# Kernel tuning notes

Measured on AMD Instinct MI355X. Metric: run time of the kernel, lower is better.

Reference implementation:

```python
import jax, jax.numpy as jnp
import numpy as np

THRESH = 230.0   # options['dist_threshold'][0]
NCAT = 21        # options['supervised_categories']


def setup_inputs() -> dict:
    key = jax.random.key(0)
    k1, k2, k3 = jax.random.split(key, 3)
    b, N, d, T = 8, 16384, 128, 64  # N = h*w = 128*128
    frame_embeddings = jax.random.normal(k1, (b, N, d), dtype=jnp.float32)
    templates = jax.random.normal(k2, (T, N, d), dtype=jnp.float32)
    template_classes = jax.random.randint(k3, (T,), 0, 20, dtype=jnp.int64)
    return {"frame_embeddings": frame_embeddings, "templates": templates,
            "template_classes": template_classes}


def _min_dists(frame_embeddings, templates):
    # frame_embeddings: [b, n, d]; templates: [t, n, d]
    x2 = jnp.sum(frame_embeddings * frame_embeddings, axis=-1)          # [b, n]
    t2 = jnp.sum(templates * templates, axis=-1)                        # [t, n]
    xt = jnp.einsum('bnd,tnd->btn', frame_embeddings, templates)        # [b, t, n]
    dists = x2[:, None, :] - 2.0 * xt + t2[None, :, :]                  # [b, t, n]
    min_d = jnp.min(dists, axis=1)                                      # [b, n]
    min_idx = jnp.argmin(dists, axis=1)                                 # [b, n]
    return min_d, min_idx


def reference(frame_embeddings, templates, template_classes):
    b, N, _ = frame_embeddings.shape
    min_d, min_idx = _min_dists(frame_embeddings, templates)
    neigh_classes = template_classes[min_idx]                           # [b, n]
    mask = min_d <= THRESH                                              # [b, n] bool
    one_hot = jax.nn.one_hot(neigh_classes, NCAT, dtype=jnp.float32)    # [b, n, ncat]
    masked_pred = one_hot * mask[:, :, None].astype(jnp.float32)        # [b, n, ncat]
    neigh_classes_masked = jnp.where(mask, neigh_classes, NCAT - 1)     # [b, n]
    return (masked_pred, mask, neigh_classes_masked, min_d, neigh_classes)
```

## Files before the change

kernel.cpp:

```cpp
#include <hip/hip_runtime.h>


#define NPIX   16384
#define DDIM   128
#define NT     64
#define NB     8
#define NCAT   21
#define THRESH 230.0f
#define P      16
#define TSTR   132

__global__ __launch_bounds__(256, 4) void nn_openset_kernel(
    const float* __restrict__ frame,
    const float* __restrict__ tmpl,
    const int*   __restrict__ tcls,
    float* __restrict__ out)
{
    __shared__ __align__(16) float ts[2][P * TSTR];

    const int tid = threadIdx.x;
    const int n0  = blockIdx.x * P;

    const int bp = tid >> 6;
    const int ln = tid & 63;
    const int np = ln >> 2;
    const int dq = ln & 3;
    const int b0 = bp * 2, b1 = b0 + 1;
    const int n  = n0 + np;

    const int r0 = tid >> 5;
    const int c0 = tid & 31;
    const int w0 = r0 * TSTR + c0 * 4;
    const int w1 = (r0 + 8) * TSTR + c0 * 4;

    const size_t PLANE4 = (size_t)NPIX * (DDIM / 4);
    const float4* gq = (const float4*)tmpl + (size_t)n0 * (DDIM / 4);

    float4 s0 = gq[tid];
    float4 s1 = gq[tid + 256];
    gq += PLANE4;

    float4 fr0[8], fr1[8];
    {
        const float4* f0 = (const float4*)(frame + ((size_t)b0 * NPIX + n) * DDIM + dq * 32);
        const float4* f1 = (const float4*)(frame + ((size_t)b1 * NPIX + n) * DDIM + dq * 32);
        #pragma unroll
        for (int j = 0; j < 8; ++j) { fr0[j] = f0[j]; fr1[j] = f1[j]; }
    }

    *(float4*)(&ts[0][w0]) = s0;
    *(float4*)(&ts[0][w1]) = s1;
    __syncthreads();

    float vmin0 = 3.402823466e38f, vmin1 = 3.402823466e38f;
    int   imin0 = 0, imin1 = 0;

    for (int t = 0; t < NT; ++t) {
        if (t < NT - 1) { s0 = gq[tid]; s1 = gq[tid + 256]; gq += PLANE4; }

        const float* tsp = &ts[t & 1][np * TSTR + dq * 32];
        float a0 = 0.0f, a1 = 0.0f;
        #pragma unroll
        for (int kq = 0; kq < 8; ++kq) {
            const float4 tv = *(const float4*)(tsp + (kq << 2));
            const float4 x0 = fr0[kq];
            const float4 x1 = fr1[kq];
            float d;
            d = x0.x - tv.x; a0 = fmaf(d, d, a0);
            d = x0.y - tv.y; a0 = fmaf(d, d, a0);
            d = x0.z - tv.z; a0 = fmaf(d, d, a0);
            d = x0.w - tv.w; a0 = fmaf(d, d, a0);
            d = x1.x - tv.x; a1 = fmaf(d, d, a1);
            d = x1.y - tv.y; a1 = fmaf(d, d, a1);
            d = x1.z - tv.z; a1 = fmaf(d, d, a1);
            d = x1.w - tv.w; a1 = fmaf(d, d, a1);
        }
        a0 += __shfl_xor(a0, 1);
        a0 += __shfl_xor(a0, 2);
        a1 += __shfl_xor(a1, 1);
        a1 += __shfl_xor(a1, 2);

        const bool u0 = a0 < vmin0;
        const bool u1 = a1 < vmin1;
        imin0 = u0 ? t : imin0;  vmin0 = u0 ? a0 : vmin0;
        imin1 = u1 ? t : imin1;  vmin1 = u1 ? a1 : vmin1;

        if (t < NT - 1) {
            float* wp = ts[(t + 1) & 1];
            *(float4*)(&wp[w0]) = s0;
            *(float4*)(&wp[w1]) = s1;
        }
        __syncthreads();
    }

    const int  cls0 = tcls[imin0];
    const int  cls1 = tcls[imin1];
    const bool m0 = (vmin0 <= THRESH);
    const bool m1 = (vmin1 <= THRESH);

    float* o0 = out;
    float* o1 = out + (size_t)NB * NPIX * NCAT;
    float* o2 = o1 + NB * NPIX;
    float* o3 = o2 + NB * NPIX;
    float* o4 = o3 + NB * NPIX;

    const size_t p0 = (size_t)b0 * NPIX + n;
    const size_t p1 = (size_t)b1 * NPIX + n;

    if (dq == 0)      { o1[p0] = m0 ? 1.0f : 0.0f;          o1[p1] = m1 ? 1.0f : 0.0f; }
    else if (dq == 1) { o2[p0] = m0 ? (float)cls0 : 20.0f;  o2[p1] = m1 ? (float)cls1 : 20.0f; }
    else if (dq == 2) { o3[p0] = vmin0;                     o3[p1] = vmin1; }
    else              { o4[p0] = (float)cls0;               o4[p1] = (float)cls1; }

    #pragma unroll
    for (int j = 0; j < 6; ++j) {
        const int c = dq * 6 + j;
        if (c < NCAT) {
            o0[p0 * NCAT + c] = (m0 && c == cls0) ? 1.0f : 0.0f;
            o0[p1 * NCAT + c] = (m1 && c == cls1) ? 1.0f : 0.0f;
        }
    }
}

extern "C" void kernel_launch(void* const* d_in, const int* in_sizes, int n_in,
                              void* d_out, int out_size, void* d_ws, size_t ws_size,
                              hipStream_t stream) {
    const float* frame = (const float*)d_in[0];
    const float* tmpl  = (const float*)d_in[1];
    const int*   tcls  = (const int*)d_in[2];
    float* outp = (float*)d_out;
    nn_openset_kernel<<<NPIX / P, 256, 0, stream>>>(frame, tmpl, tcls, outp);
}
```

Measured before the change: 710.0 us.

## Stream templates into LDS via async global_load_lds with 4-stage ring buffer

Replaces the register-staged double-buffered template copy with direct global-to-LDS DMA loads (global_load_lds) into a 4-deep ring buffer, prefetching three templates ahead. An XOR swizzle on the source column replaces the padded stride to avoid LDS bank conflicts, and explicit vmcnt waits plus raw s_barrier replace __syncthreads. This aims to hide global-memory latency and cut the VGPR traffic of staging loads, at the cost of more LDS (32KB per block), which may limit occupancy, and fragile hand-tuned waitcnt counts.

```diff
diff --git a/kernel.cpp b/kernel.cpp
--- a/kernel.cpp
+++ b/kernel.cpp
@@ -8,7 +8,15 @@
 #define NCAT   21
 #define THRESH 230.0f
 #define P      16
-#define TSTR   132
+
+typedef float4 f4;
+
+__device__ __forceinline__ void dma16(const float* g, float* l) {
+    __builtin_amdgcn_global_load_lds(
+        (const __attribute__((address_space(1))) void*)g,
+        (__attribute__((address_space(3))) void*)l,
+        16 , 0, 0);
+}
 
 __global__ __launch_bounds__(256, 4) void nn_openset_kernel(
     const float* __restrict__ frame,
@@ -16,7 +24,7 @@
     const int*   __restrict__ tcls,
     float* __restrict__ out)
 {
-    __shared__ __align__(16) float ts[2][P * TSTR];
+    __shared__ __align__(16) float ts[4][P * DDIM];
 
     const int tid = threadIdx.x;
     const int n0  = blockIdx.x * P;
@@ -27,44 +35,58 @@
     const int dq = ln & 3;
     const int b0 = bp * 2, b1 = b0 + 1;
     const int n  = n0 + np;
+    const int wv = __builtin_amdgcn_readfirstlane(bp);
 
-    const int r0 = tid >> 5;
-    const int c0 = tid & 31;
-    const int w0 = r0 * TSTR + c0 * 4;
-    const int w1 = (r0 + 8) * TSTR + c0 * 4;
-
-    const size_t PLANE4 = (size_t)NPIX * (DDIM / 4);
-    const float4* gq = (const float4*)tmpl + (size_t)n0 * (DDIM / 4);
-
-    float4 s0 = gq[tid];
-    float4 s1 = gq[tid + 256];
-    gq += PLANE4;
-
-    float4 fr0[8], fr1[8];
+    f4 fr0[8], fr1[8];
     {
-        const float4* f0 = (const float4*)(frame + ((size_t)b0 * NPIX + n) * DDIM + dq * 32);
-        const float4* f1 = (const float4*)(frame + ((size_t)b1 * NPIX + n) * DDIM + dq * 32);
+        const f4* f0 = (const f4*)(frame + ((size_t)b0 * NPIX + n) * DDIM + dq * 32);
+        const f4* f1 = (const f4*)(frame + ((size_t)b1 * NPIX + n) * DDIM + dq * 32);
         #pragma unroll
         for (int j = 0; j < 8; ++j) { fr0[j] = f0[j]; fr1[j] = f1[j]; }
     }
 
-    *(float4*)(&ts[0][w0]) = s0;
-    *(float4*)(&ts[0][w1]) = s1;
-    __syncthreads();
+    const size_t PLANE = (size_t)NPIX * DDIM;
+    const int c0  = tid;
+    const int c1  = tid + 256;
+    const int sc0 = c0 ^ ((c0 >> 5) & 7);
+    const int sc1 = c1 ^ ((c1 >> 5) & 7);
+    const float* gp0 = tmpl + (size_t)n0 * DDIM + sc0 * 4;
+    const float* gp1 = tmpl + (size_t)n0 * DDIM + sc1 * 4;
+    const int ldso0 = wv * 256;
+    const int ldso1 = 1024 + wv * 256;
+
+    dma16(gp0,             &ts[0][ldso0]);  dma16(gp1,             &ts[0][ldso1]);
+    dma16(gp0 + PLANE,     &ts[1][ldso0]);  dma16(gp1 + PLANE,     &ts[1][ldso1]);
+    dma16(gp0 + 2 * PLANE, &ts[2][ldso0]);  dma16(gp1 + 2 * PLANE, &ts[2][ldso1]);
+    gp0 += 3 * PLANE;  gp1 += 3 * PLANE;
+
+    const int s  = np & 7;
+    const int rb = np * DDIM + dq * 32;
+    int roff[8];
+    #pragma unroll
+    for (int kq = 0; kq < 8; ++kq) roff[kq] = rb + ((kq ^ s) << 2);
+
+    asm volatile("s_waitcnt vmcnt(4)" ::: "memory");
+    __builtin_amdgcn_s_barrier();
 
     float vmin0 = 3.402823466e38f, vmin1 = 3.402823466e38f;
     int   imin0 = 0, imin1 = 0;
 
     for (int t = 0; t < NT; ++t) {
-        if (t < NT - 1) { s0 = gq[tid]; s1 = gq[tid + 256]; gq += PLANE4; }
+        if (t + 3 < NT) {
+            float* wb = ts[(t + 3) & 3];
+            dma16(gp0, wb + ldso0);
+            dma16(gp1, wb + ldso1);
+            gp0 += PLANE;  gp1 += PLANE;
+        }
 
-        const float* tsp = &ts[t & 1][np * TSTR + dq * 32];
+        const float* tb = ts[t & 3];
         float a0 = 0.0f, a1 = 0.0f;
         #pragma unroll
         for (int kq = 0; kq < 8; ++kq) {
-            const float4 tv = *(const float4*)(tsp + (kq << 2));
-            const float4 x0 = fr0[kq];
-            const float4 x1 = fr1[kq];
+            const f4 tv = *(const f4*)(tb + roff[kq]);
+            const f4 x0 = fr0[kq];
+            const f4 x1 = fr1[kq];
             float d;
             d = x0.x - tv.x; a0 = fmaf(d, d, a0);
             d = x0.y - tv.y; a0 = fmaf(d, d, a0);
@@ -75,10 +97,8 @@
             d = x1.z - tv.z; a1 = fmaf(d, d, a1);
             d = x1.w - tv.w; a1 = fmaf(d, d, a1);
         }
-        a0 += __shfl_xor(a0, 1);
-        a0 += __shfl_xor(a0, 2);
-        a1 += __shfl_xor(a1, 1);
-        a1 += __shfl_xor(a1, 2);
+        a0 += __shfl_xor(a0, 1);  a0 += __shfl_xor(a0, 2);
+        a1 += __shfl_xor(a1, 1);  a1 += __shfl_xor(a1, 2);
 
         const bool u0 = a0 < vmin0;
         const bool u1 = a1 < vmin1;
@@ -86,11 +106,11 @@
         imin1 = u1 ? t : imin1;  vmin1 = u1 ? a1 : vmin1;
 
         if (t < NT - 1) {
-            float* wp = ts[(t + 1) & 1];
-            *(float4*)(&wp[w0]) = s0;
-            *(float4*)(&wp[w1]) = s1;
+            if (t < NT - 3)       asm volatile("s_waitcnt vmcnt(4)" ::: "memory");
+            else if (t == NT - 3) asm volatile("s_waitcnt vmcnt(2)" ::: "memory");
+            else                  asm volatile("s_waitcnt vmcnt(0)" ::: "memory");
+            __builtin_amdgcn_s_barrier();
         }
-        __syncthreads();
     }
 
     const int  cls0 = tcls[imin0];
```

Result: no change. 717.5 us (+1.0%).

## Drop LDS template staging; load templates directly from global per thread

Applied to the files above, without the earlier changes.

Removes the double-buffered shared-memory staging of template rows and the per-iteration block barrier. The thread mapping changes so that the four batch lanes sharing a pixel read the same template data directly from global memory, relying on L1/L2 broadcast. This removes synchronisation and LDS traffic but gives up explicit prefetch overlap, and it raises register pressure by holding 8 float4 template values per iteration.

```diff
diff --git a/kernel.cpp b/kernel.cpp
--- a/kernel.cpp
+++ b/kernel.cpp
@@ -8,7 +8,8 @@
 #define NCAT   21
 #define THRESH 230.0f
 #define P      16
-#define TSTR   132
+
+typedef float4 f4;
 
 __global__ __launch_bounds__(256, 4) void nn_openset_kernel(
     const float* __restrict__ frame,
@@ -16,81 +17,60 @@
     const int*   __restrict__ tcls,
     float* __restrict__ out)
 {
-    __shared__ __align__(16) float ts[2][P * TSTR];
-
     const int tid = threadIdx.x;
     const int n0  = blockIdx.x * P;
 
-    const int bp = tid >> 6;
+    const int wv = tid >> 6;
     const int ln = tid & 63;
-    const int np = ln >> 2;
+    const int np = ln >> 4;
+    const int b  = (ln >> 2) & 3;
     const int dq = ln & 3;
-    const int b0 = bp * 2, b1 = b0 + 1;
-    const int n  = n0 + np;
+    const int n  = n0 + wv * 4 + np;
+    const int b0 = b, b1 = b + 4;
 
-    const int r0 = tid >> 5;
-    const int c0 = tid & 31;
-    const int w0 = r0 * TSTR + c0 * 4;
-    const int w1 = (r0 + 8) * TSTR + c0 * 4;
-
-    const size_t PLANE4 = (size_t)NPIX * (DDIM / 4);
-    const float4* gq = (const float4*)tmpl + (size_t)n0 * (DDIM / 4);
-
-    float4 s0 = gq[tid];
-    float4 s1 = gq[tid + 256];
-    gq += PLANE4;
-
-    float4 fr0[8], fr1[8];
+    f4 fr0[8], fr1[8];
     {
-        const float4* f0 = (const float4*)(frame + ((size_t)b0 * NPIX + n) * DDIM + dq * 32);
-        const float4* f1 = (const float4*)(frame + ((size_t)b1 * NPIX + n) * DDIM + dq * 32);
+        const f4* f0 = (const f4*)(frame + ((size_t)b0 * NPIX + n) * DDIM + dq * 32);
+        const f4* f1 = (const f4*)(frame + ((size_t)b1 * NPIX + n) * DDIM + dq * 32);
         #pragma unroll
         for (int j = 0; j < 8; ++j) { fr0[j] = f0[j]; fr1[j] = f1[j]; }
     }
 
-    *(float4*)(&ts[0][w0]) = s0;
-    *(float4*)(&ts[0][w1]) = s1;
-    __syncthreads();
+    const size_t PLANE4 = (size_t)NPIX * (DDIM / 4);
+    const f4* tp = (const f4*)tmpl + (size_t)n * (DDIM / 4) + dq * 8;
 
     float vmin0 = 3.402823466e38f, vmin1 = 3.402823466e38f;
     int   imin0 = 0, imin1 = 0;
 
     for (int t = 0; t < NT; ++t) {
-        if (t < NT - 1) { s0 = gq[tid]; s1 = gq[tid + 256]; gq += PLANE4; }
+        f4 tv[8];
+        #pragma unroll
+        for (int kq = 0; kq < 8; ++kq) tv[kq] = tp[kq];
+        tp += PLANE4;
 
-        const float* tsp = &ts[t & 1][np * TSTR + dq * 32];
         float a0 = 0.0f, a1 = 0.0f;
         #pragma unroll
         for (int kq = 0; kq < 8; ++kq) {
-            const float4 tv = *(const float4*)(tsp + (kq << 2));
-            const float4 x0 = fr0[kq];
-            const float4 x1 = fr1[kq];
+            const f4 v  = tv[kq];
+            const f4 x0 = fr0[kq];
+            const f4 x1 = fr1[kq];
             float d;
-            d = x0.x - tv.x; a0 = fmaf(d, d, a0);
-            d = x0.y - tv.y; a0 = fmaf(d, d, a0);
-            d = x0.z - tv.z; a0 = fmaf(d, d, a0);
-            d = x0.w - tv.w; a0 = fmaf(d, d, a0);
-            d = x1.x - tv.x; a1 = fmaf(d, d, a1);
-            d = x1.y - tv.y; a1 = fmaf(d, d, a1);
-            d = x1.z - tv.z; a1 = fmaf(d, d, a1);
-            d = x1.w - tv.w; a1 = fmaf(d, d, a1);
+            d = x0.x - v.x; a0 = fmaf(d, d, a0);
+            d = x0.y - v.y; a0 = fmaf(d, d, a0);
+            d = x0.z - v.z; a0 = fmaf(d, d, a0);
+            d = x0.w - v.w; a0 = fmaf(d, d, a0);
+            d = x1.x - v.x; a1 = fmaf(d, d, a1);
+            d = x1.y - v.y; a1 = fmaf(d, d, a1);
+            d = x1.z - v.z; a1 = fmaf(d, d, a1);
+            d = x1.w - v.w; a1 = fmaf(d, d, a1);
         }
-        a0 += __shfl_xor(a0, 1);
-        a0 += __shfl_xor(a0, 2);
-        a1 += __shfl_xor(a1, 1);
-        a1 += __shfl_xor(a1, 2);
+        a0 += __shfl_xor(a0, 1);  a0 += __shfl_xor(a0, 2);
+        a1 += __shfl_xor(a1, 1);  a1 += __shfl_xor(a1, 2);
 
         const bool u0 = a0 < vmin0;
         const bool u1 = a1 < vmin1;
         imin0 = u0 ? t : imin0;  vmin0 = u0 ? a0 : vmin0;
         imin1 = u1 ? t : imin1;  vmin1 = u1 ? a1 : vmin1;
-
-        if (t < NT - 1) {
-            float* wp = ts[(t + 1) & 1];
-            *(float4*)(&wp[w0]) = s0;
-            *(float4*)(&wp[w1]) = s1;
-        }
-        __syncthreads();
     }
 
     const int  cls0 = tcls[imin0];
```

Measured after the change: 809.9 us. 1.14x slower.
